# Kernel tuning notes

Hardware: AMD Instinct MI355X
Metric: run time of the kernel (lower is better)

The kernel has to match this reference:

```python
import jax, jax.numpy as jnp
import numpy as np

B, T, V = 256, 40, 5000
D, Z, L = 512, 128, 2


def setup_inputs() -> dict:
    key = jax.random.key(0)
    ks = jax.random.split(key, 10)
    s = 0.05  # weight scale to keep gates unsaturated
    return {
        "z": jax.random.normal(ks[0], (B, Z), jnp.float32),
        "x": jax.random.randint(ks[1], (B, T), 0, V),
        "emb": jax.random.normal(ks[2], (V, D), jnp.float32) * s,
        "Wg0": jax.random.normal(ks[3], (4, D, D + Z + D), jnp.float32) * s,
        "bg0": jnp.zeros((4, D), jnp.float32),
        "Wg1": jax.random.normal(ks[4], (4, D, D + D), jnp.float32) * s,
        "bg1": jnp.zeros((4, D), jnp.float32),
        "Wout": jax.random.normal(ks[5], (V, D + Z), jnp.float32) * s,
        "bout": jnp.zeros((V,), jnp.float32),
        "tw1": jax.random.normal(ks[6], (L, 4 * D, Z), jnp.float32) * s,
        "tb1": jnp.zeros((L, 4 * D), jnp.float32),
        "tw2": jax.random.normal(ks[7], (L, 2 * D, 4 * D), jnp.float32) * s,
        "tb2": jnp.zeros((L, 2 * D), jnp.float32),
    }


def reference(z, x, emb, Wg0, bg0, Wg1, bg1, Wout, bout, tw1, tb1, tw2, tb2):
    b, d = z.shape[0], emb.shape[1]
    # transformh0: Linear -> ReLU -> Linear -> Tanh, then split into (h0, c0)
    states = []
    for l in range(L):
        hh = jnp.tanh(jax.nn.relu(z @ tw1[l].T + tb1[l]) @ tw2[l].T + tb2[l])
        hh = hh.reshape(b, 2, d)
        states.append((hh[:, 0], hh[:, 1]))
    states = tuple(states)

    emb_x = emb[x]  # [B, T, D]
    Ws, bs = (Wg0, Wg1), (bg0, bg1)

    def cell(xin, h, c, W, bb):
        hx = jnp.concatenate([h, xin], axis=-1)  # Gate cats [h, input]
        g = jnp.einsum('bf,gdf->bgd', hx, W) + bb  # fused 4 gate GEMMs
        i = jax.nn.sigmoid(g[:, 0])
        f = jax.nn.sigmoid(g[:, 1])
        o = jax.nn.sigmoid(g[:, 2])
        cn = jnp.tanh(g[:, 3])
        c = f * c + i * cn
        return o * jnp.tanh(c), c

    def multi(xin, states):
        H = jnp.zeros((b, d), xin.dtype)
        new, cur = [], xin
        for l in range(L):
            h, c = cell(cur, states[l][0], states[l][1], Ws[l], bs[l])
            H = H + h
            new.append((h, c))
            cur = h
        return H, tuple(new)

    h_t, states = multi(jnp.concatenate([emb_x[:, 0], z], axis=-1), states)

    def step(carry, inp):
        h_t, states = carry
        e_i, x_i = inp
        logits = jnp.concatenate([h_t, z], axis=-1) @ Wout.T + bout
        lp = jax.nn.log_softmax(logits, axis=-1)
        lp_i = jnp.take_along_axis(lp, x_i[:, None], axis=-1)  # [B,1]
        h_t, states = multi(jnp.concatenate([e_i, z], axis=-1), states)
        return (h_t, states), lp_i

    xs = (jnp.swapaxes(emb_x[:, 1:], 0, 1), x[:, 1:].T)
    _, lps = jax.lax.scan(step, (h_t, states), xs)
    # cumsum over time then take last == sum over steps -> [B, 1]
    return jnp.sum(lps, axis=0)
```

## Files before the change

### kernel.cpp

```cpp
#include <hip/hip_runtime.h>


typedef unsigned int uint;
typedef unsigned short ushort;
typedef unsigned long long u64;
typedef __attribute__((ext_vector_type(8))) __bf16 bf16x8;
typedef __attribute__((ext_vector_type(4))) float f32x4;
typedef __attribute__((ext_vector_type(8))) ushort ushort8v;

#define OFF_CNT 0L
#define OFF_W0  4096L
#define OFF_W1  4722688L
#define OFF_WO  8916992L
#define OFF_EFT 15470592L
#define OFF_ZFT 25956352L
#define OFF_TW1 26021888L
#define OFF_TW2 27070464L
#define OFF_GB  35459072L
#define OFF_C0  40701952L
#define OFF_C1  41226240L
#define OFF_MB  41750528L
#define OFF_SB  41914368L
#define OFF_TGT 42078208L
#define OFF_H0S 42205184L
#define OFF_H1S 52690944L
#define OFF_HSS 63176704L

#define HPAR 262144L
#define HMT  131072L
#define SLOT_G 24576
#define SLOT_L 32768


__device__ __forceinline__ uint ald32(const uint* p) {
  return __hip_atomic_load(p, __ATOMIC_RELAXED, __HIP_MEMORY_SCOPE_AGENT);
}
__device__ __forceinline__ void ast32(uint* p, uint v) {
  __hip_atomic_store(p, v, __ATOMIC_RELAXED, __HIP_MEMORY_SCOPE_AGENT);
}
__device__ __forceinline__ float aldf(const float* p) {
  return __hip_atomic_load(p, __ATOMIC_RELAXED, __HIP_MEMORY_SCOPE_AGENT);
}
__device__ __forceinline__ void astf(float* p, float v) {
  __hip_atomic_store(p, v, __ATOMIC_RELAXED, __HIP_MEMORY_SCOPE_AGENT);
}
__device__ __forceinline__ void ast64(u64* p, u64 v) {
  __hip_atomic_store(p, v, __ATOMIC_RELAXED, __HIP_MEMORY_SCOPE_AGENT);
}

__device__ __forceinline__ void postS(uint* s, uint v) {
  __syncthreads();
  if (threadIdx.x == 0) ast32(s, v);
}

__device__ __forceinline__ void gateM(const uint* S, int n, u64 need, uint tgt, uint& vc) {
  if (threadIdx.x < 64) {
    const int li = threadIdx.x;
    uint v = (li < n) ? vc : 0xffffffffu;
    int r = 0;
    for (;;) {
      if ((__ballot((int)(v >= tgt)) & need) == need) break;
      if (li < n && v < tgt) v = ald32(S + li);
      if ((__ballot((int)(v >= tgt)) & need) == need) break;
      if (r < 2) __builtin_amdgcn_s_sleep(1);
      else if (r < 5) __builtin_amdgcn_s_sleep(4);
      else __builtin_amdgcn_s_sleep(8);
      ++r;
    }
    if (li < n) vc = v;
  }
  asm volatile("" ::: "memory");
  __builtin_amdgcn_s_barrier();
  asm volatile("" ::: "memory");
}

__device__ __forceinline__ ushort f2bf(float f) {
  uint u = __float_as_uint(f);
  u = (u + 0x7fffu + ((u >> 16) & 1u)) >> 16;
  return (ushort)u;
}
__device__ __forceinline__ float bf2f(ushort u) { return __uint_as_float(((uint)u) << 16); }
__device__ __forceinline__ float sigm(float v) { return 1.f / (1.f + __expf(-v)); }
__device__ __forceinline__ float tanh_f(float v) {
  float a = fabsf(v);
  float e = __expf(-2.f * a);
  return copysignf((1.f - e) / (1.f + e), v);
}
__device__ __forceinline__ f32x4 mfma16(bf16x8 a, bf16x8 b, f32x4 c) {
  return __builtin_amdgcn_mfma_f32_16x16x32_bf16(a, b, c, 0, 0, 0);
}

__device__ __forceinline__ long fta(int b, int k, int KC) {
  return ((long)(((b >> 7) & 1) * KC + (k >> 5)) << 12) +
         (((((b >> 4) & 7) << 2) + ((k >> 3) & 3)) << 7) + ((b & 15) << 3) + (k & 7);
}

__device__ __forceinline__ void gl_lds16(const char* g, char* l) {
  __builtin_amdgcn_global_load_lds((const __attribute__((address_space(1))) void*)g,
                                   (__attribute__((address_space(3))) void*)l, 16, 0, 0);
}

__device__ __forceinline__ void stageA4(const char* A, char* dst, int o) {
#pragma unroll
  for (int i = 0; i < 4; ++i) gl_lds16(A + i * 4096 + o, dst + i * 4096 + o);
}
__device__ __forceinline__ void stage_gB(int bsec, const char* Bs, char* dst, int o) {
  const char* B = Bs + (long)bsec * 8192;
#pragma unroll
  for (int i = 0; i < 2; ++i) gl_lds16(B + i * 4096 + o, dst + 16384 + i * 4096 + o);
}
__device__ __forceinline__ void stage_lB(int bsec, const char* Blo, const char* Bhi, char* dst,
                                         int o) {
  const char* bl = Blo + (long)bsec * 8192;
  const char* bh = Bhi + (long)bsec * 8192;
#pragma unroll
  for (int i = 0; i < 2; ++i) gl_lds16(bl + i * 4096 + o, dst + 16384 + i * 4096 + o);
#pragma unroll
  for (int i = 0; i < 2; ++i) gl_lds16(bh + i * 4096 + o, dst + 24576 + i * 4096 + o);
}

__device__ __forceinline__ void gw3(int r) {
  if (r <= 0) __builtin_amdgcn_s_waitcnt(0x0F70);
  else if (r == 1) __builtin_amdgcn_s_waitcnt(0x0F76);
  else if (r == 2) __builtin_amdgcn_s_waitcnt(0x0F7C);
  else __builtin_amdgcn_s_waitcnt(0x4F72);
}
__device__ __forceinline__ void lw2(int r) {
  if (r <= 0) __builtin_amdgcn_s_waitcnt(0x0F70);
  else if (r == 1) __builtin_amdgcn_s_waitcnt(0x0F78);
  else __builtin_amdgcn_s_waitcnt(0x4F70);
}

__device__ __forceinline__ void gemm_chunk_g(const char* sb, int ab, int bb, f32x4 (&acc)[4][2]) {
#pragma unroll
  for (int c = 0; c < 2; ++c) {
    const char* ap = sb + c * 8192 + ab;
    const char* bp = sb + c * 4096 + bb;
    bf16x8 Af0 = *(const bf16x8*)(ap);
    bf16x8 Af1 = *(const bf16x8*)(ap + 1024);
    bf16x8 Af2 = *(const bf16x8*)(ap + 2048);
    bf16x8 Af3 = *(const bf16x8*)(ap + 3072);
    bf16x8 Bf0 = *(const bf16x8*)(bp);
    bf16x8 Bf1 = *(const bf16x8*)(bp + 1024);
    acc[0][0] = mfma16(Af0, Bf0, acc[0][0]);
    acc[0][1] = mfma16(Af0, Bf1, acc[0][1]);
    acc[1][0] = mfma16(Af1, Bf0, acc[1][0]);
    acc[1][1] = mfma16(Af1, Bf1, acc[1][1]);
    acc[2][0] = mfma16(Af2, Bf0, acc[2][0]);
    acc[2][1] = mfma16(Af2, Bf1, acc[2][1]);
    acc[3][0] = mfma16(Af3, Bf0, acc[3][0]);
    acc[3][1] = mfma16(Af3, Bf1, acc[3][1]);
  }
}

__device__ __forceinline__ void gemm_chunk_l(const char* sb, int ab, int bb, f32x4 (&acc)[4][4]) {
#pragma unroll
  for (int c = 0; c < 2; ++c) {
    const char* ap = sb + c * 8192 + ab;
    const char* bp = sb + c * 4096 + bb;
    bf16x8 Af[4], Bf[4];
#pragma unroll
    for (int m = 0; m < 4; ++m) Af[m] = *(const bf16x8*)(ap + m * 1024);
#pragma unroll
    for (int n = 0; n < 4; ++n) Bf[n] = *(const bf16x8*)(bp + n * 1024);
#pragma unroll
    for (int m = 0; m < 4; ++m)
#pragma unroll
      for (int n = 0; n < 4; ++n) acc[m][n] = mfma16(Af[m], Bf[n], acc[m][n]);
  }
}

__device__ __forceinline__ void phaseG8(const char* A0, const char* Bs, int bsec0, char* smem,
                                        int o, int ab, int bb, f32x4 (&acc)[4][2]) {
#pragma unroll
  for (int p = 0; p < 5; ++p) {
    char* d = smem + p * SLOT_G;
    stageA4(A0 + (long)p * 16384, d, o);
    stage_gB(bsec0 + p, Bs, d, o);
  }
#pragma unroll
  for (int s = 0; s < 8; ++s) {
    if (s == 0) __builtin_amdgcn_s_waitcnt(0x4F78);
    else if (s <= 4) __builtin_amdgcn_s_waitcnt(0x4F72);
    else if (s == 5) __builtin_amdgcn_s_waitcnt(0x0F7C);
    else if (s == 6) __builtin_amdgcn_s_waitcnt(0x0F76);
    else __builtin_amdgcn_s_waitcnt(0x0F70);
    __builtin_amdgcn_s_barrier();
    if (s >= 1 && s <= 3) {
      const int sn = s + 4;
      char* d = smem + (sn % 5) * SLOT_G;
      stageA4(A0 + (long)sn * 16384, d, o);
      stage_gB(bsec0 + sn, Bs, d, o);
    }
    gemm_chunk_g(smem + (s % 5) * SLOT_G, ab, bb, acc);
  }
  __builtin_amdgcn_s_barrier();
}

__device__ __forceinline__ void phaseL8(const char* A0, const char* Blo, const char* Bhi,
                                        char* smem, int o, int ab, int bb, f32x4 (&acc)[4][4]) {
#pragma unroll
  for (int p = 0; p < 4; ++p) {
    char* d = smem + p * SLOT_L;
    stageA4(A0 + (long)p * 16384, d, o);
    stage_lB(p, Blo, Bhi, d, o);
  }
#pragma unroll
  for (int s = 0; s < 8; ++s) {
    if (s == 0) __builtin_amdgcn_s_waitcnt(0x4F78);
    else if (s <= 5) __builtin_amdgcn_s_waitcnt(0x4F70);
    else if (s == 6) __builtin_amdgcn_s_waitcnt(0x0F78);
    else __builtin_amdgcn_s_waitcnt(0x0F70);
    __builtin_amdgcn_s_barrier();
    if (s >= 1 && s <= 4) {
      const int sn = s + 3;
      char* d = smem + (sn % 4) * SLOT_L;
      stageA4(A0 + (long)sn * 16384, d, o);
      stage_lB(sn, Blo, Bhi, d, o);
    }
    gemm_chunk_l(smem + (s % 4) * SLOT_L, ab, bb, acc);
  }
  __builtin_amdgcn_s_barrier();
}

__device__ __forceinline__ void run_gemm_init(const char* A0, const char* Bs, int S, char* smem,
                                              int tid, int wm, int wn, int lane,
                                              f32x4 (&acc)[4][2]) {
  const int o = tid * 16;
  const int D = S < 4 ? S : 4;
  for (int s = 0; s < D; ++s) {
    char* d = smem + s * SLOT_G;
    stageA4(A0 + (long)s * 16384, d, o);
    stage_gB(s, Bs, d, o);
  }
  const int ab = wm * 4096 + lane * 16;
  const int bb = 16384 + wn * 2048 + lane * 16;
  for (int s = 0; s < S; ++s) {
    const int rem = S - 1 - s;
    gw3(rem < 3 ? rem : 3);
    __builtin_amdgcn_s_barrier();
    char* sb = smem + (s % 5) * SLOT_G;
    if (s + 4 < S) {
      char* d = smem + ((s + 4) % 5) * SLOT_G;
      stageA4(A0 + (long)(s + 4) * 16384, d, o);
      stage_gB(s + 4, Bs, d, o);
    }
    gemm_chunk_g(sb, ab, bb, acc);
  }
  __syncthreads();
}

__device__ __forceinline__ void store_lds_tile(float* lds, f32x4 (&acc)[4][2], int wm, int wn,
                                               int lane) {
  const int l15 = lane & 15, lq = lane >> 4;
#pragma unroll
  for (int m = 0; m < 4; ++m)
#pragma unroll
    for (int n = 0; n < 2; ++n)
#pragma unroll
      for (int r = 0; r < 4; ++r)
        lds[(wm * 64 + m * 16 + lq * 4 + r) * 68 + (wn * 32 + n * 16 + l15)] = acc[m][n][r];
}
__device__ __forceinline__ void store_lds_tile128(float* lds, f32x4 (&acc)[4][4], int wm, int wn,
                                                  int lane) {
  const int l15 = lane & 15, lq = lane >> 4;
#pragma unroll
  for (int m = 0; m < 4; ++m)
#pragma unroll
    for (int n = 0; n < 4; ++n)
#pragma unroll
      for (int r = 0; r < 4; ++r)
        lds[(wm * 64 + m * 16 + lq * 4 + r) * 132 + (wn * 64 + n * 16 + l15)] = acc[m][n][r];
}

template <bool WHS>
__device__ __forceinline__ void gates_pw4(const float* tile, int tid, int b0, int d0,
                                          const float* __restrict__ bg, float (&cp)[8],
                                          ushort* __restrict__ hw, const uint (&h0p)[4],
                                          ushort* __restrict__ hs) {
#pragma unroll
  for (int jj = 0; jj < 4; ++jj) {
    const int pi = tid + jj * 256;
    const int bl = pi >> 3, e = pi & 7;
    const f32x4 g0 = ((const f32x4*)tile)[bl * 17 + 2 * e];
    const f32x4 g1 = ((const f32x4*)tile)[bl * 17 + 2 * e + 1];
    const int d = d0 + 2 * e, b = b0 + bl;
    float h2[2];
#pragma unroll
    for (int u = 0; u < 2; ++u) {
      const f32x4 g = u ? g1 : g0;
      const int dd = d + u;
      const float ii = sigm(g[0] + bg[dd]);
      const float ff = sigm(g[1] + bg[512 + dd]);
      const float oo = sigm(g[2] + bg[1024 + dd]);
      const float cn = tanh_f(g[3] + bg[1536 + dd]);
      const float c = ff * cp[jj * 2 + u] + ii * cn;
      cp[jj * 2 + u] = c;
      h2[u] = oo * tanh_f(c);
    }
    const long ft = fta(b, d, 16);
    ast32((uint*)(hw + ft), (uint)f2bf(h2[0]) | ((uint)f2bf(h2[1]) << 16));
    if (WHS) {
      const uint h0v = h0p[jj];
      const float s0 = h2[0] + bf2f((ushort)(h0v & 0xffffu));
      const float s1 = h2[1] + bf2f((ushort)(h0v >> 16));
      ast32((uint*)(hs + ft), (uint)f2bf(s0) | ((uint)f2bf(s1) << 16));
    }
  }
}

__device__ __forceinline__ float combine_row4(const float* __restrict__ MBc,
                                              const float* __restrict__ SBc,
                                              const float* __restrict__ TGTc, int r, int lane) {
  float M = lane < 40 ? aldf(&MBc[r * 40 + lane]) : -3.0e38f;
  float S = lane < 40 ? aldf(&SBc[r * 40 + lane]) : 0.f;
#pragma unroll
  for (int off = 32; off > 0; off >>= 1) {
    const float Mo = __shfl_xor(M, off, 64);
    const float So = __shfl_xor(S, off, 64);
    const float Mn = fmaxf(M, Mo);
    S = S * __expf(M - Mn) + So * __expf(Mo - Mn);
    M = Mn;
  }
  return aldf(&TGTc[r]) - (M + __logf(S));
}

__device__ __forceinline__ void cv8(ushort8v& o, const float* s) {
  const f32x4 a = *(const f32x4*)s, b = *(const f32x4*)(s + 4);
#pragma unroll
  for (int j = 0; j < 4; ++j) o[j] = f2bf(a[j]);
#pragma unroll
  for (int j = 0; j < 4; ++j) o[4 + j] = f2bf(b[j]);
}
__device__ __forceinline__ void bft8(ushort* dst, int col, int kg, int KC, const float* src) {
  ushort8v o;
  cv8(o, src);
  *(ushort8v*)(dst + ((long)((col >> 6) * KC + (kg >> 2)) << 11) +
               (((((col >> 4) & 3) << 2) + (kg & 3)) << 7) + ((col & 15) << 3)) = o;
}
__device__ __forceinline__ void bft8z(ushort* dst, int col, int kg, int KC) {
  ushort8v o = (ushort8v)0;
  *(ushort8v*)(dst + ((long)((col >> 6) * KC + (kg >> 2)) << 11) +
               (((((col >> 4) & 3) << 2) + (kg & 3)) << 7) + ((col & 15) << 3)) = o;
}
__device__ __forceinline__ void aft8(ushort* dst, int b, int kg, int KC, const float* src) {
  ushort8v o;
  cv8(o, src);
  *(ushort8v*)(dst + ((long)(((b >> 7) & 1) * KC + (kg >> 2)) << 12) +
               (((((b >> 4) & 7) << 2) + (kg & 3)) << 7) + ((b & 15) << 3)) = o;
}

__global__ void __launch_bounds__(256) prep_kernel(
    const float* __restrict__ Wg0, const float* __restrict__ Wg1, const float* __restrict__ Wout,
    const float* __restrict__ emb, const float* __restrict__ z, const int* __restrict__ x,
    const float* __restrict__ tw1, const float* __restrict__ tw2, unsigned char* __restrict__ ws) {
  ushort* W0 = (ushort*)(ws + OFF_W0);
  ushort* W1 = (ushort*)(ws + OFF_W1);
  ushort* WO = (ushort*)(ws + OFF_WO);
  ushort* EF = (ushort*)(ws + OFF_EFT);
  ushort* ZF = (ushort*)(ws + OFF_ZFT);
  ushort* T1 = (ushort*)(ws + OFF_TW1);
  ushort* T2 = (ushort*)(ws + OFF_TW2);
  const long N0 = 294912, N1 = 262144, N2 = 409600, N3 = 655360, N4 = 4096, N5 = 65536,
             N6 = 524288;
  const long total = N0 + N1 + N2 + N3 + N4 + N5 + N6;
  for (long idx = (long)blockIdx.x * 256 + threadIdx.x; idx < total;
       idx += (long)gridDim.x * 256) {
    long j = idx;
    if (j < N0) {
      const int col = (int)(j / 144), kg = (int)(j - (long)col * 144);
      bft8(W0, col, kg, 36, Wg0 + (long)((col & 3) * 512 + (col >> 2)) * 1152 + kg * 8);
    } else if ((j -= N0) < N1) {
      const int col = (int)(j >> 7), kg = (int)(j & 127);
      bft8(W1, col, kg, 32, Wg1 + (long)((col & 3) * 512 + (col >> 2)) * 1024 + kg * 8);
    } else if ((j -= N1) < N2) {
      const int col = (int)(j / 80), kg = (int)(j - (long)col * 80);
      if (col < 5000)
        bft8(WO, col, kg, 20, Wout + (long)col * 640 + kg * 8);
      else
        bft8z(WO, col, kg, 20);
    } else if ((j -= N2) < N3) {
      const int t = (int)(j >> 14), r = (int)(j & 16383);
      const int b = r >> 6, kg = r & 63;
      aft8(EF + (long)t * 131072, b, kg, 16, emb + (long)x[b * 40 + t] * 512 + kg * 8);
    } else if ((j -= N3) < N4) {
      const int b = (int)(j >> 4), kg = (int)(j & 15);
      aft8(ZF, b, kg, 4, z + b * 128 + kg * 8);
    } else if ((j -= N4) < N5) {
      const int col = (int)(j >> 4), kg = (int)(j & 15);
      bft8(T1, col, kg, 4, tw1 + (long)(col >> 11) * 262144 + (long)(col & 2047) * 128 + kg * 8);
    } else {
      j -= N5;
      const int col = (int)(j >> 8), kg = (int)(j & 255);
      bft8(T2, col, kg, 64, tw2 + (long)(col >> 10) * 2097152 + (long)(col & 1023) * 2048 + kg * 8);
    }
  }
}

__global__ void __launch_bounds__(256) decoder_main(
    const int* __restrict__ x, const float* __restrict__ bg0, const float* __restrict__ bg1,
    const float* __restrict__ bout, const float* __restrict__ tb1, const float* __restrict__ tb2,
    unsigned char* __restrict__ ws, float* __restrict__ out) {
  __shared__ __align__(16) char smem[157696];

  uint* CNT = (uint*)(ws + OFF_CNT);

  const char* cW0 = (const char*)(ws + OFF_W0);
  const char* cW1 = (const char*)(ws + OFF_W1);
  const char* cWO = (const char*)(ws + OFF_WO);
  const char* cEF = (const char*)(ws + OFF_EFT);
  const char* cZF = (const char*)(ws + OFF_ZFT);
  const char* cT1 = (const char*)(ws + OFF_TW1);
  const char* cT2 = (const char*)(ws + OFF_TW2);
  char* cGB = (char*)(ws + OFF_GB);
  char* cH0S = (char*)(ws + OFF_H0S);
  char* cH1S = (char*)(ws + OFF_H1S);
  char* cHSS = (char*)(ws + OFF_HSS);
  float* C0f = (float*)(ws + OFF_C0);
  float* C1f = (float*)(ws + OFF_C1);
  float* MBf = (float*)(ws + OFF_MB);
  float* SBf = (float*)(ws + OFF_SB);
  float* TGTf = (float*)(ws + OFF_TGT);

  const int bid = blockIdx.x;
  const int tid = threadIdx.x;
  const int lane = tid & 63;
  const int w = tid >> 6;
  const int wm = w & 1, wn = w >> 1;
  const int xcd = bid & 7;
  const int slot = bid >> 3;
  const int o16 = tid * 16;

  int role, mt_r = 0, idx = 0;
  if (xcd < 2) {
    role = 0; mt_r = xcd; idx = slot;
  } else if (xcd < 4) {
    role = 1; mt_r = xcd - 2; idx = slot;
  } else if (xcd < 6) {
    role = 2; mt_r = xcd - 4; idx = slot;
  } else if (slot < 8) {
    role = 2; mt_r = xcd - 6; idx = 32 + slot;
  } else if (slot < 24) {
    role = 3; idx = (xcd - 6) * 16 + (slot - 8); mt_r = idx >> 4;
  } else {
    return;
  }

  const int ab = wm * 4096 + lane * 16;
  const int bbg = 16384 + wn * 2048 + lane * 16;
  const int bbl = 16384 + wn * 8192 + lane * 16;
  float* EPI = (float*)(smem + 122880);

  float cpriv[8];
  float accO0 = 0.f, accO1 = 0.f;

  if (bid < 128) {
    const int i_mt = bid & 1, i_ng = bid >> 1;
    f32x4 acc[4][2];
#pragma unroll
    for (int m = 0; m < 4; ++m)
#pragma unroll
      for (int n = 0; n < 2; ++n) acc[m][n] = (f32x4){0.f, 0.f, 0.f, 0.f};
    run_gemm_init(cZF + (long)i_mt * 32768, cT1 + (long)i_ng * 16384, 2, smem, tid, wm, wn,
                  lane, acc);
    store_lds_tile(EPI, acc, wm, wn, lane);
    __syncthreads();
    const int b0i = i_mt * 128, n0i = i_ng * 64;
    ushort* GBu = (ushort*)cGB;
    for (int i = tid; i < 2048; i += 256) {
      const int bl = i >> 4, q = i & 15;
      const f32x4 v = ((const f32x4*)EPI)[bl * 17 + q];
      const int cb = n0i + q * 4;
      const int l = cb >> 11, rr = cb & 2047;
      u64 pk = 0;
#pragma unroll
      for (int cc = 0; cc < 4; ++cc) pk |= (u64)f2bf(fmaxf(v[cc] + tb1[cb + cc], 0.f)) << (cc * 16);
      ast64((u64*)(GBu + (long)l * 524288 + fta(b0i + bl, rr, 64)), pk);
    }
    postS(CNT + 512 + bid, 1u);
  }

  if (bid < 64) {
    uint ca = 0, cb2 = 0;
    gateM(CNT + 512, 64, ~0ull, 1u, ca);
    gateM(CNT + 576, 64, ~0ull, 1u, cb2);
    const int i_mt = bid & 1, i_ng = bid >> 1;
    const int l = i_ng >> 4;
    f32x4 acc[4][2];
#pragma unroll
    for (int m = 0; m < 4; ++m)
#pragma unroll
      for (int n = 0; n < 2; ++n) acc[m][n] = (f32x4){0.f, 0.f, 0.f, 0.f};
    run_gemm_init(cGB + (long)l * 1048576 + (long)i_mt * 524288, cT2 + (long)i_ng * 262144, 32,
                  smem, tid, wm, wn, lane, acc);
    store_lds_tile(EPI, acc, wm, wn, lane);
    __syncthreads();
    const int b0i = i_mt * 128, n0i = i_ng * 64;
    for (int i = tid; i < 2048; i += 256) {
      const int bl = i >> 4, q = i & 15;
      const f32x4 v = ((const f32x4*)EPI)[bl * 17 + q];
      const int cb = n0i + q * 4;
      const int ll = cb >> 10, rr = cb & 1023;
      const int b = b0i + bl;
      if (rr < 512) {
        u64 pk = 0;
#pragma unroll
        for (int cc = 0; cc < 4; ++cc) pk |= (u64)f2bf(tanh_f(v[cc] + tb2[cb + cc])) << (cc * 16);
        ast64((u64*)((ushort*)(ll ? cH1S : cH0S) + fta(b, rr, 16)), pk);
      } else {
        float* Cf = (ll ? C1f : C0f) + b * 512 + (rr - 512);
#pragma unroll
        for (int cc = 0; cc < 4; ++cc) astf(Cf + cc, tanh_f(v[cc] + tb2[cb + cc]));
      }
    }
    postS(CNT + 640 + bid, 1u);
  }

  if (role == 0) {
    const int mt = mt_r, g = idx;
    uint* SH0m = CNT + mt * 64;
    const char* Az = cZF + (long)mt * 32768;
    const char* Bs = cW0 + (long)g * 147456;
    f32x4 pz0[4][2];
#pragma unroll
    for (int m = 0; m < 4; ++m)
#pragma unroll
      for (int n = 0; n < 2; ++n) pz0[m][n] = (f32x4){0.f, 0.f, 0.f, 0.f};
    run_gemm_init(Az, Bs + 131072, 2, smem, tid, wm, wn, lane, pz0);
    uint cI2 = 0, ch0 = 0;
    gateM(CNT + 640, 64, ~0ull, 1u, cI2);
#pragma unroll
    for (int jj = 0; jj < 4; ++jj) {
      const int pi = tid + jj * 256, bl = pi >> 3, e = pi & 7;
      cpriv[jj * 2 + 0] = aldf(&C0f[(mt * 128 + bl) * 512 + g * 16 + 2 * e]);
      cpriv[jj * 2 + 1] = aldf(&C0f[(mt * 128 + bl) * 512 + g * 16 + 2 * e + 1]);
    }
    uint dum[4] = {0, 0, 0, 0};
    for (int t = 0; t < 39; ++t) {
      const char* Ae = cEF + (long)t * HPAR + (long)mt * HMT;
      const char* Ah = cH0S + (long)t * HPAR + (long)mt * HMT;
      f32x4 acc[4][2];
#pragma unroll
      for (int m = 0; m < 4; ++m)
#pragma unroll
        for (int n = 0; n < 2; ++n) acc[m][n] = pz0[m][n];
      phaseG8(Ae, Bs, 8, smem, o16, ab, bbg, acc);
      if (t >= 1) gateM(SH0m, 32, 0xFFFFFFFFull, (uint)t, ch0);
      phaseG8(Ah, Bs, 0, smem, o16, ab, bbg, acc);
      store_lds_tile(EPI, acc, wm, wn, lane);
      __syncthreads();
      gates_pw4<false>(EPI, tid, mt * 128, g * 16, bg0, cpriv,
                       (ushort*)(cH0S + (long)(t + 1) * HPAR), dum, nullptr);
      postS(&SH0m[g], (uint)(t + 1));
    }
  } else if (role == 1) {
    const int mt = mt_r, g = idx;
    uint* SH0m = CNT + mt * 64;
    uint* SH1m = CNT + 128 + mt * 64;
    const char* Bs = cW1 + (long)g * 131072;
    uint cI2 = 0, ch1 = 0, ch0 = 0;
    gateM(CNT + 640, 64, ~0ull, 1u, cI2);
#pragma unroll
    for (int jj = 0; jj < 4; ++jj) {
      const int pi = tid + jj * 256, bl = pi >> 3, e = pi & 7;
      cpriv[jj * 2 + 0] = aldf(&C1f[(mt * 128 + bl) * 512 + g * 16 + 2 * e]);
      cpriv[jj * 2 + 1] = aldf(&C1f[(mt * 128 + bl) * 512 + g * 16 + 2 * e + 1]);
    }
    for (int t = 0; t < 39; ++t) {
      const char* Ah1 = cH1S + (long)t * HPAR + (long)mt * HMT;
      const char* Ah0 = cH0S + (long)(t + 1) * HPAR + (long)mt * HMT;
      if (t >= 1) gateM(SH1m, 32, 0xFFFFFFFFull, (uint)t, ch1);
      f32x4 acc[4][2];
#pragma unroll
      for (int m = 0; m < 4; ++m)
#pragma unroll
        for (int n = 0; n < 2; ++n) acc[m][n] = (f32x4){0.f, 0.f, 0.f, 0.f};
      phaseG8(Ah1, Bs, 0, smem, o16, ab, bbg, acc);
      gateM(SH0m, 32, 0xFFFFFFFFull, (uint)(t + 1), ch0);
      uint h0p[4];
      {
        const ushort* h0r = (const ushort*)(cH0S + (long)(t + 1) * HPAR);
#pragma unroll
        for (int jj = 0; jj < 4; ++jj) {
          const int pi = tid + jj * 256, bl = pi >> 3, e = pi & 7;
          h0p[jj] = *(const uint*)(h0r + fta(mt * 128 + bl, g * 16 + 2 * e, 16));
        }
      }
      phaseG8(Ah0, Bs, 8, smem, o16, ab, bbg, acc);
      store_lds_tile(EPI, acc, wm, wn, lane);
      __syncthreads();
      gates_pw4<true>(EPI, tid, mt * 128, g * 16, bg1, cpriv,
                      (ushort*)(cH1S + (long)(t + 1) * HPAR), h0p,
                      (ushort*)(cHSS + (long)t * HPAR));
      postS(&SH1m[g], (uint)(t + 1));
    }
  } else if (role == 2) {
    const int lmt = mt_r, lng = idx;
    uint* SH1m = CNT + 128 + lmt * 64;
    uint* SLGm = CNT + 256 + lmt * 64;
    uint* SCBm = CNT + 384 + lmt * 64;
    const char* Blo = cWO + (long)(2 * lng) * 81920;
    const char* Bhi = cWO + (long)(2 * lng + 1) * 81920;
    const char* Az = cZF + (long)lmt * 32768;
    f32x4 pz[4][4];
#pragma unroll
    for (int m = 0; m < 4; ++m)
#pragma unroll
      for (int n = 0; n < 4; ++n) pz[m][n] = (f32x4){0.f, 0.f, 0.f, 0.f};
#pragma unroll
    for (int p = 0; p < 2; ++p) {
      char* d = smem + p * SLOT_L;
      stageA4(Az + (long)p * 16384, d, o16);
      stage_lB(8 + p, Blo, Bhi, d, o16);
    }
    for (int s = 0; s < 2; ++s) {
      lw2(1 - s);
      __builtin_amdgcn_s_barrier();
      gemm_chunk_l(smem + s * SLOT_L, ab, bbl, pz);
    }
    __syncthreads();
    {
      const int l15 = lane & 15;
#pragma unroll
      for (int n = 0; n < 4; ++n) {
        const int col = lng * 128 + wn * 64 + n * 16 + l15;
        const float bb = col < 5000 ? bout[col] : -3.0e38f;
#pragma unroll
        for (int m = 0; m < 4; ++m)
#pragma unroll
          for (int r = 0; r < 4; ++r) pz[m][n][r] += bb;
      }
    }
    uint ch1 = 0, ccb = 0;
    for (int t = 0; t < 39; ++t) {
      const char* Ahs = cHSS + (long)t * HPAR + (long)lmt * HMT;
      if (t >= 4) gateM(SCBm, 16, 0xFFFFull, (uint)(t - 3), ccb);
      gateM(SH1m, 32, 0xFFFFFFFFull, (uint)(t + 1), ch1);
      f32x4 acc[4][4];
#pragma unroll
      for (int m = 0; m < 4; ++m)
#pragma unroll
        for (int n = 0; n < 4; ++n) acc[m][n] = pz[m][n];
      phaseL8(Ahs, Blo, Bhi, smem, o16, ab, bbl, acc);
      __syncthreads();
      store_lds_tile128((float*)smem, acc, wm, wn, lane);
      __syncthreads();
      const int row = tid >> 1, half = tid & 1, b = lmt * 128 + row;
      const int n0 = lng * 128 + half * 64;
      const int xt = x[b * 40 + t + 1];
      const float* rowp = (const float*)smem + row * 132 + half * 64;
      float mx = -3.0e38f, tv = 0.f;
      for (int j = 0; j < 64; j += 4) {
        const f32x4 v = *(const f32x4*)(rowp + j);
#pragma unroll
        for (int cc = 0; cc < 4; ++cc) {
          mx = fmaxf(mx, v[cc]);
          if (n0 + j + cc == xt) tv = v[cc];
        }
      }
      float sa = 0.f;
      for (int j = 0; j < 64; j += 4) {
        const f32x4 v = *(const f32x4*)(rowp + j);
#pragma unroll
        for (int cc = 0; cc < 4; ++cc) sa += __expf(v[cc] - mx);
      }
      const float mo = __shfl_xor(mx, 1, 64), so = __shfl_xor(sa, 1, 64),
                  to = __shfl_xor(tv, 1, 64);
      const float Mn = fmaxf(mx, mo);
      const float Sm = sa * __expf(mx - Mn) + so * __expf(mo - Mn);
      const int sl = t & 3;
      if (half == 0) {
        astf(&MBf[sl * 10240 + b * 40 + lng], Mn);
        astf(&SBf[sl * 10240 + b * 40 + lng], Sm);
        if (xt >= lng * 128 && xt < lng * 128 + 128) astf(&TGTf[sl * 256 + b], tv + to);
      }
      postS(&SLGm[lng], (uint)(t + 1));
    }
  } else {
    const int cb = idx;
    const int cmt = mt_r;
    uint* SLGm = CNT + 256 + cmt * 64;
    uint* SCBm = CNT + 384 + cmt * 64;
    const int r0 = cb * 8 + w * 2;
    uint clg = 0;
    for (int t = 0; t < 39; ++t) {
      gateM(SLGm, 40, (1ull << 40) - 1, (uint)(t + 1), clg);
      const int sl = t & 3;
      accO0 += combine_row4(MBf + sl * 10240, SBf + sl * 10240, TGTf + sl * 256, r0, lane);
      accO1 += combine_row4(MBf + sl * 10240, SBf + sl * 10240, TGTf + sl * 256, r0 + 1, lane);
      postS(&SCBm[cb & 15], (uint)(t + 1));
    }
    if (lane == 0) {
      out[r0] = accO0;
      out[r0 + 1] = accO1;
    }
  }
}

extern "C" void kernel_launch(void* const* d_in, const int* in_sizes, int n_in, void* d_out,
                              int out_size, void* d_ws, size_t ws_size, hipStream_t stream) {
  const float* z = (const float*)d_in[0];
  const int* x = (const int*)d_in[1];
  const float* emb = (const float*)d_in[2];
  const float* Wg0 = (const float*)d_in[3];
  const float* bg0 = (const float*)d_in[4];
  const float* Wg1 = (const float*)d_in[5];
  const float* bg1 = (const float*)d_in[6];
  const float* Wout = (const float*)d_in[7];
  const float* bout = (const float*)d_in[8];
  const float* tw1 = (const float*)d_in[9];
  const float* tb1 = (const float*)d_in[10];
  const float* tw2 = (const float*)d_in[11];
  const float* tb2 = (const float*)d_in[12];
  unsigned char* ws = (unsigned char*)d_ws;
  float* out = (float*)d_out;

  hipMemsetAsync(ws, 0, 4096, stream);
  prep_kernel<<<2048, 256, 0, stream>>>(Wg0, Wg1, Wout, emb, z, x, tw1, tw2, ws);
  decoder_main<<<256, 256, 0, stream>>>(x, bg0, bg1, bout, tb1, tb2, ws, out);
}
```

Baseline: 617.6 us.

## Merge the two K-phase gate GEMMs into one continuous 16-stage pipeline

The two 8-stage phases of each LSTM layer's gate GEMM (input part and recurrent part) are replaced by a single 16-stage loop with a 5-slot LDS ring. Prefetch now carries on across the boundary between the two operand halves, so the pipeline no longer drains and refills in the middle. To allow this, the wait on the previous layer's hidden-state flag (gateM) is moved ahead of the whole GEMM. That removes the overlap the old code had between the first phase and the inter-block dependency wait, and may lengthen the critical path of the recurrence.

```diff
diff --git a/kernel.cpp b/kernel.cpp
--- a/kernel.cpp
+++ b/kernel.cpp
@@ -130,6 +130,13 @@
   else if (r == 1) __builtin_amdgcn_s_waitcnt(0x0F78);
   else __builtin_amdgcn_s_waitcnt(0x4F70);
 }
+__device__ __forceinline__ void gvw16(int s) {
+  if (s == 0) __builtin_amdgcn_s_waitcnt(0x4F78);
+  else if (s <= 12) __builtin_amdgcn_s_waitcnt(0x4F72);
+  else if (s == 13) __builtin_amdgcn_s_waitcnt(0x0F7C);
+  else if (s == 14) __builtin_amdgcn_s_waitcnt(0x0F76);
+  else __builtin_amdgcn_s_waitcnt(0x0F70);
+}
 
 __device__ __forceinline__ void gemm_chunk_g(const char* sb, int ab, int bb, f32x4 (&acc)[4][2]) {
 #pragma unroll
@@ -168,33 +175,6 @@
 #pragma unroll
       for (int n = 0; n < 4; ++n) acc[m][n] = mfma16(Af[m], Bf[n], acc[m][n]);
   }
-}
-
-__device__ __forceinline__ void phaseG8(const char* A0, const char* Bs, int bsec0, char* smem,
-                                        int o, int ab, int bb, f32x4 (&acc)[4][2]) {
-#pragma unroll
-  for (int p = 0; p < 5; ++p) {
-    char* d = smem + p * SLOT_G;
-    stageA4(A0 + (long)p * 16384, d, o);
-    stage_gB(bsec0 + p, Bs, d, o);
-  }
-#pragma unroll
-  for (int s = 0; s < 8; ++s) {
-    if (s == 0) __builtin_amdgcn_s_waitcnt(0x4F78);
-    else if (s <= 4) __builtin_amdgcn_s_waitcnt(0x4F72);
-    else if (s == 5) __builtin_amdgcn_s_waitcnt(0x0F7C);
-    else if (s == 6) __builtin_amdgcn_s_waitcnt(0x0F76);
-    else __builtin_amdgcn_s_waitcnt(0x0F70);
-    __builtin_amdgcn_s_barrier();
-    if (s >= 1 && s <= 3) {
-      const int sn = s + 4;
-      char* d = smem + (sn % 5) * SLOT_G;
-      stageA4(A0 + (long)sn * 16384, d, o);
-      stage_gB(bsec0 + sn, Bs, d, o);
-    }
-    gemm_chunk_g(smem + (s % 5) * SLOT_G, ab, bb, acc);
-  }
-  __builtin_amdgcn_s_barrier();
 }
 
 __device__ __forceinline__ void phaseL8(const char* A0, const char* Blo, const char* Bhi,
@@ -539,14 +519,34 @@
     for (int t = 0; t < 39; ++t) {
       const char* Ae = cEF + (long)t * HPAR + (long)mt * HMT;
       const char* Ah = cH0S + (long)t * HPAR + (long)mt * HMT;
+      if (t >= 1) gateM(SH0m, 32, 0xFFFFFFFFull, (uint)t, ch0);
       f32x4 acc[4][2];
 #pragma unroll
       for (int m = 0; m < 4; ++m)
 #pragma unroll
         for (int n = 0; n < 2; ++n) acc[m][n] = pz0[m][n];
-      phaseG8(Ae, Bs, 8, smem, o16, ab, bbg, acc);
-      if (t >= 1) gateM(SH0m, 32, 0xFFFFFFFFull, (uint)t, ch0);
-      phaseG8(Ah, Bs, 0, smem, o16, ab, bbg, acc);
+#pragma unroll
+      for (int p = 0; p < 5; ++p) {
+        char* d = smem + p * SLOT_G;
+        stageA4(Ae + (long)p * 16384, d, o16);
+        stage_gB(8 + p, Bs, d, o16);
+      }
+      for (int s = 0; s < 16; ++s) {
+        gvw16(s);
+        __builtin_amdgcn_s_barrier();
+        const int sn = s + 4;
+        if (s >= 1 && sn < 16) {
+          char* d = smem + (sn % 5) * SLOT_G;
+          if (sn < 8) {
+            stageA4(Ae + (long)sn * 16384, d, o16);
+            stage_gB(8 + sn, Bs, d, o16);
+          } else {
+            stageA4(Ah + (long)(sn - 8) * 16384, d, o16);
+            stage_gB(sn - 8, Bs, d, o16);
+          }
+        }
+        gemm_chunk_g(smem + (s % 5) * SLOT_G, ab, bbg, acc);
+      }
       store_lds_tile(EPI, acc, wm, wn, lane);
       __syncthreads();
       gates_pw4<false>(EPI, tid, mt * 128, g * 16, bg0, cpriv,
@@ -570,13 +570,30 @@
       const char* Ah1 = cH1S + (long)t * HPAR + (long)mt * HMT;
       const char* Ah0 = cH0S + (long)(t + 1) * HPAR + (long)mt * HMT;
       if (t >= 1) gateM(SH1m, 32, 0xFFFFFFFFull, (uint)t, ch1);
+      gateM(SH0m, 32, 0xFFFFFFFFull, (uint)(t + 1), ch0);
       f32x4 acc[4][2];
 #pragma unroll
       for (int m = 0; m < 4; ++m)
 #pragma unroll
         for (int n = 0; n < 2; ++n) acc[m][n] = (f32x4){0.f, 0.f, 0.f, 0.f};
-      phaseG8(Ah1, Bs, 0, smem, o16, ab, bbg, acc);
-      gateM(SH0m, 32, 0xFFFFFFFFull, (uint)(t + 1), ch0);
+#pragma unroll
+      for (int p = 0; p < 5; ++p) {
+        char* d = smem + p * SLOT_G;
+        stageA4(Ah1 + (long)p * 16384, d, o16);
+        stage_gB(p, Bs, d, o16);
+      }
+      for (int s = 0; s < 16; ++s) {
+        gvw16(s);
+        __builtin_amdgcn_s_barrier();
+        const int sn = s + 4;
+        if (s >= 1 && sn < 16) {
+          char* d = smem + (sn % 5) * SLOT_G;
+          const char* A = sn < 8 ? Ah1 + (long)sn * 16384 : Ah0 + (long)(sn - 8) * 16384;
+          stageA4(A, d, o16);
+          stage_gB(sn, Bs, d, o16);
+        }
+        gemm_chunk_g(smem + (s % 5) * SLOT_G, ab, bbg, acc);
+      }
       uint h0p[4];
       {
         const ushort* h0r = (const ushort*)(cH0S + (long)(t + 1) * HPAR);
@@ -586,7 +603,6 @@
           h0p[jj] = *(const uint*)(h0r + fta(mt * 128 + bl, g * 16 + 2 * e, 16));
         }
       }
-      phaseG8(Ah0, Bs, 8, smem, o16, ab, bbg, acc);
       store_lds_tile(EPI, acc, wm, wn, lane);
       __syncthreads();
       gates_pw4<true>(EPI, tid, mt * 128, g * 16, bg1, cpriv,
```

New measurement: 580.6 us. -6.0%, faster.
